# Optimization experiments

Hardware: AMD Instinct MI355X
Metric: run time of the kernel (lower is better)

## Reference

```python
import jax, jax.numpy as jnp
import numpy as np

B, C, D = 8192, 10000, 128
CLAMP_MIN, CLAMP_MAX = 1e-12, 1e12


def setup_inputs() -> dict:
    key = jax.random.key(0)
    k1, k2, k3 = jax.random.split(key, 3)
    x = jax.random.normal(k1, (B, D), dtype=jnp.float32)
    labels = jax.random.randint(k2, (B,), 0, C, dtype=jnp.int64)
    centers = jax.random.normal(k3, (C, D), dtype=jnp.float32)
    lr = jnp.array([0.1], dtype=jnp.float32)
    return {"x": x, "labels": labels, "centers": centers, "lr": lr}


def reference(x, labels, centers, lr):
    b, d = x.shape
    c = centers.shape[0]
    # --- vectorized center update (replaces double python loop) ---
    # A_j = count_j * centers[j] - sum_{i: labels_i==j} x_i ; delta_j = A_j / (1 + count_j)
    counts = jax.ops.segment_sum(jnp.ones((b,), dtype=x.dtype), labels, num_segments=c)  # [C]
    sum_x = jax.ops.segment_sum(x, labels, num_segments=c)                               # [C, D]
    delta = (counts[:, None] * centers - sum_x) / (1.0 + counts[:, None])
    centers = centers - lr * delta
    # --- squared euclidean distance matrix [B, C] ---
    distmat = (
        jnp.sum(x * x, axis=1, keepdims=True)
        + jnp.sum(centers * centers, axis=1)[None, :]
        - 2.0 * (x @ centers.T)
    )
    git = 1.0 / (1.0 + distmat)
    # gather own-class entries (replaces per-sample mask loop)
    lab = labels[:, None]
    center_vals = jnp.take_along_axis(distmat, lab, axis=1)[:, 0]          # [B]
    git_vals = jnp.sum(git, axis=1) - jnp.take_along_axis(git, lab, axis=1)[:, 0]
    center_loss = jnp.mean(jnp.clip(center_vals, CLAMP_MIN, CLAMP_MAX))
    git_loss = jnp.mean(jnp.clip(git_vals, CLAMP_MIN, CLAMP_MAX))
    return (center_loss, git_loss)
```

## Files before the change

### kernel.cpp

```cpp
#include <hip/hip_runtime.h>
#include <hip/hip_bf16.h>

#define B_ 8192
#define C_ 10000
#define D_ 128
#define CPAD 10112
#define NPADC 112
#define NT_TOT 158
#define NSTRIP 16
#define STRIPW 10

typedef float f32x4 __attribute__((ext_vector_type(4)));
typedef short s16x8 __attribute__((ext_vector_type(8)));

typedef const __attribute__((address_space(1))) uint32_t gu32;
typedef __attribute__((address_space(3))) uint32_t lu32;


__global__ void scatter_xprep(const float* __restrict__ x, const int* __restrict__ labels,
                              float* __restrict__ counts, float* __restrict__ sumx,
                              float* __restrict__ xnorm, __hip_bfloat16* __restrict__ xb) {
    int tid = threadIdx.x;
    int w = tid >> 6, lane = tid & 63;
    int i = blockIdx.x * 4 + w;
    int l = labels[i];
    float2 v = *(const float2*)&x[i * D_ + lane * 2];
    atomicAdd(&sumx[l * D_ + lane * 2], v.x);
    atomicAdd(&sumx[l * D_ + lane * 2 + 1], v.y);
    if (lane == 0) atomicAdd(&counts[l], 1.0f);
    __hip_bfloat162 p;
    p.x = __float2bfloat16(v.x);
    p.y = __float2bfloat16(v.y);
    *(__hip_bfloat162*)&xb[i * D_ + lane * 2] = p;
    float s = v.x * v.x + v.y * v.y;
    #pragma unroll
    for (int m = 1; m < 64; m <<= 1) s += __shfl_xor(s, m);
    if (lane == 0) xnorm[i] = s;
}

__global__ void center_update(const float* __restrict__ centers, const float* __restrict__ counts,
                              float* __restrict__ sumx_cnew, float* __restrict__ cnorm,
                              __hip_bfloat16* __restrict__ cb, const float* __restrict__ lr) {
    int tid = threadIdx.x;
    int w = tid >> 6, lane = tid & 63;
    int c = blockIdx.x * 4 + w;
    if (c >= C_) {
        *(uint*)&cb[c * D_ + lane * 2] = 0u;
        if (lane == 0) cnorm[c] = 0.0f;
        return;
    }
    float cnt = counts[c];
    float lrv = lr[0];
    float2 cv = *(const float2*)&centers[c * D_ + lane * 2];
    float2 sx = *(const float2*)&sumx_cnew[c * D_ + lane * 2];
    float inv = 1.0f / (1.0f + cnt);
    float nx = cv.x - lrv * (cnt * cv.x - sx.x) * inv;
    float ny = cv.y - lrv * (cnt * cv.y - sx.y) * inv;
    float2 nn = {nx, ny};
    *(float2*)&sumx_cnew[c * D_ + lane * 2] = nn;
    __hip_bfloat162 p;
    p.x = __float2bfloat16(nx);
    p.y = __float2bfloat16(ny);
    *(__hip_bfloat162*)&cb[c * D_ + lane * 2] = p;
    float s = nx * nx + ny * ny;
    #pragma unroll
    for (int m = 1; m < 64; m <<= 1) s += __shfl_xor(s, m);
    if (lane == 0) cnorm[c] = s;
}

__global__ void center_vals_k(const float* __restrict__ x, const int* __restrict__ labels,
                              const float* __restrict__ cnew, float* __restrict__ cent_val) {
    int tid = threadIdx.x;
    int w = tid >> 6, lane = tid & 63;
    int i = blockIdx.x * 4 + w;
    int l = labels[i];
    float2 a = *(const float2*)&x[i * D_ + lane * 2];
    float2 c = *(const float2*)&cnew[l * D_ + lane * 2];
    float dx = a.x - c.x, dy = a.y - c.y;
    float s = dx * dx + dy * dy;
    #pragma unroll
    for (int m = 1; m < 64; m <<= 1) s += __shfl_xor(s, m);
    if (lane == 0) cent_val[i] = s;
}

__global__ void __launch_bounds__(512)
gemm_git(const __hip_bfloat16* __restrict__ xb, const __hip_bfloat16* __restrict__ cb,
         const float* __restrict__ xnorm, const float* __restrict__ cnorm,
         float* __restrict__ git_row) {
    __shared__ char ldsB[2][16384];

    int tid = threadIdx.x;
    int w = tid >> 6, lane = tid & 63;
    int lr_ = lane & 15, lg = lane >> 4;
    int strip = blockIdx.x;
    int bm = blockIdx.y;
    int row0 = bm * 512 + w * 64;
    int bn0 = strip * STRIPW;
    int nt = (strip == NSTRIP - 1) ? (NT_TOT - bn0) : STRIPW;

    const s16x8* gx = (const s16x8*)xb;

    s16x8 af[4][4];
    #pragma unroll
    for (int kk = 0; kk < 4; kk++)
        #pragma unroll
        for (int f = 0; f < 4; f++)
            af[kk][f] = gx[(row0 + f * 16 + lr_) * 16 + kk * 4 + lg];

    float xn1[4][4];
    #pragma unroll
    for (int fm = 0; fm < 4; fm++)
        #pragma unroll
        for (int r = 0; r < 4; r++)
            xn1[fm][r] = 1.0f + xnorm[row0 + fm * 16 + lg * 4 + r];

    float gitsum[4][4] = {};

    const char* gB = (const char*)cb;
    int sr0 = tid >> 4,          sc0 = (tid & 15) ^ (sr0 & 7);
    int sr1 = (tid + 512) >> 4,  sc1 = ((tid + 512) & 15) ^ (sr1 & 7);
    size_t goff0 = (size_t)(sr0 * 16 + sc0) * 16;
    size_t goff1 = (size_t)(sr1 * 16 + sc1) * 16;

    auto stage = [&](int t, int buf) {
        const char* base = gB + (size_t)(bn0 + t) * 64 * 256;
        __builtin_amdgcn_global_load_lds((gu32*)(base + goff0),
                                         (lu32*)&ldsB[buf][tid * 16], 16, 0, 0);
        __builtin_amdgcn_global_load_lds((gu32*)(base + goff1),
                                         (lu32*)&ldsB[buf][8192 + tid * 16], 16, 0, 0);
    };

    stage(0, 0);
    __syncthreads();

    int cur = 0;
    for (int t = 0; t < nt; ++t) {
        if (t + 1 < nt) stage(t + 1, cur ^ 1);

        int cb0 = (bn0 + t) * 64;
        float cn[4];
        #pragma unroll
        for (int fn = 0; fn < 4; fn++) cn[fn] = cnorm[cb0 + fn * 16 + lr_];

        f32x4 acc[4][4] = {};
        #pragma unroll
        for (int kk = 0; kk < 4; kk++) {
            s16x8 bfk[4];
            int kc = kk * 4 + lg;
            #pragma unroll
            for (int fn = 0; fn < 4; fn++) {
                int row = fn * 16 + lr_;
                int ch = kc ^ (lr_ & 7);
                bfk[fn] = *(const s16x8*)&ldsB[cur][(row * 16 + ch) * 16];
            }
            #pragma unroll
            for (int fm = 0; fm < 4; fm++)
                #pragma unroll
                for (int fn = 0; fn < 4; fn++)
                    acc[fm][fn] = __builtin_amdgcn_mfma_f32_16x16x32_bf16(af[kk][fm], bfk[fn], acc[fm][fn], 0, 0, 0);
        }

        #pragma unroll
        for (int fm = 0; fm < 4; fm++)
            #pragma unroll
            for (int r = 0; r < 4; r++) {
                float base = xn1[fm][r];
                #pragma unroll
                for (int fp = 0; fp < 4; fp += 2) {
                    float u = base + cn[fp]     - 2.0f * acc[fm][fp][r];
                    float v = base + cn[fp + 1] - 2.0f * acc[fm][fp + 1][r];
                    gitsum[fm][r] += (u + v) * __builtin_amdgcn_rcpf(u * v);
                }
            }

        __syncthreads();
        cur ^= 1;
    }

    #pragma unroll
    for (int fm = 0; fm < 4; fm++)
        #pragma unroll
        for (int r = 0; r < 4; r++) {
            float s = gitsum[fm][r];
            s += __shfl_xor(s, 1); s += __shfl_xor(s, 2);
            s += __shfl_xor(s, 4); s += __shfl_xor(s, 8);
            if (lr_ == 0) atomicAdd(&git_row[row0 + fm * 16 + lg * 4 + r], s);
        }
}

__global__ void final_reduce(const float* __restrict__ cent_val, const float* __restrict__ git_row,
                             const float* __restrict__ xnorm, float* __restrict__ out) {
    int tid = threadIdx.x;
    int w = tid >> 6, lane = tid & 63;
    float cl = 0.0f, gl = 0.0f;
    #pragma unroll
    for (int j = 0; j < 2; j++) {
        int base = (tid * 2 + j) * 4;
        float4 cv = *(const float4*)&cent_val[base];
        float4 gr = *(const float4*)&git_row[base];
        float4 xn = *(const float4*)&xnorm[base];
        float cvs[4] = {cv.x, cv.y, cv.z, cv.w};
        float grs[4] = {gr.x, gr.y, gr.z, gr.w};
        float xns[4] = {xn.x, xn.y, xn.z, xn.w};
        #pragma unroll
        for (int e = 0; e < 4; e++) {
            float c = cvs[e];
            cl += fminf(fmaxf(c, 1e-12f), 1e12f);
            float g = grs[e] - 1.0f / (1.0f + c) - (float)NPADC / (1.0f + xns[e]);
            gl += fminf(fmaxf(g, 1e-12f), 1e12f);
        }
    }
    #pragma unroll
    for (int m = 1; m < 64; m <<= 1) { cl += __shfl_xor(cl, m); gl += __shfl_xor(gl, m); }
    __shared__ float scl[16], sgl[16];
    if (lane == 0) { scl[w] = cl; sgl[w] = gl; }
    __syncthreads();
    if (tid == 0) {
        float a = 0.0f, b = 0.0f;
        #pragma unroll
        for (int k = 0; k < 16; k++) { a += scl[k]; b += sgl[k]; }
        out[0] = a / (float)B_;
        out[1] = b / (float)B_;
    }
}

extern "C" void kernel_launch(void* const* d_in, const int* in_sizes, int n_in,
                              void* d_out, int out_size, void* d_ws, size_t ws_size,
                              hipStream_t stream) {
    const float* x       = (const float*)d_in[0];
    const int*   labels  = (const int*)d_in[1];
    const float* centers = (const float*)d_in[2];
    const float* lr      = (const float*)d_in[3];

    float* ws       = (float*)d_ws;
    float* counts   = ws;
    float* sumx     = ws + 10240;
    float* git_row  = ws + 1290240;
    float* xnorm    = ws + 1298432;
    float* cent_val = ws + 1306624;
    float* cnorm    = ws + 1314816;
    __hip_bfloat16* xb = (__hip_bfloat16*)((char*)d_ws + 5300224);
    __hip_bfloat16* cb = (__hip_bfloat16*)((char*)d_ws + 7397376);
    float* out = (float*)d_out;

    hipMemsetAsync(d_ws, 0, (size_t)1298432 * 4, stream);

    scatter_xprep<<<B_ / 4, 256, 0, stream>>>(x, labels, counts, sumx, xnorm, xb);
    center_update<<<CPAD / 4, 256, 0, stream>>>(centers, counts, sumx, cnorm, cb, lr);
    center_vals_k<<<B_ / 4, 256, 0, stream>>>(x, labels, sumx, cent_val);
    gemm_git<<<dim3(NSTRIP, 16), 512, 0, stream>>>(xb, cb, xnorm, cnorm, git_row);
    final_reduce<<<1, 1024, 0, stream>>>(cent_val, git_row, xnorm, out);
}
```

Measured before the change: 57.58 us.

## Fuse center update with own-class distances and shrink GEMM blocks

Merges the center-update and own-class distance kernels into one launch, with the distance blocks recomputing the updated center directly from centers, counts and sumx. This removes one kernel launch and one round trip through global memory. The GEMM blocks drop from 512 to 256 threads, which doubles the number of blocks on the grid to improve occupancy and load balance. The memset is replaced by a zeroing kernel, and the final reduction is spread over 32 blocks that combine results with atomics, which adds atomic accumulation into the output.

```diff
diff --git a/kernel.cpp b/kernel.cpp
--- a/kernel.cpp
+++ b/kernel.cpp
@@ -9,6 +9,8 @@
 #define NT_TOT 158
 #define NSTRIP 16
 #define STRIPW 10
+#define UPD_BLOCKS 2528
+#define CVAL_BLOCKS 2048
 
 typedef float f32x4 __attribute__((ext_vector_type(4)));
 typedef short s16x8 __attribute__((ext_vector_type(8)));
@@ -16,6 +18,11 @@
 typedef const __attribute__((address_space(1))) uint32_t gu32;
 typedef __attribute__((address_space(3))) uint32_t lu32;
 
+
+__global__ void zero_ws(float4* __restrict__ ws, float* __restrict__ out) {
+    ws[blockIdx.x * 256 + threadIdx.x] = float4{0.f, 0.f, 0.f, 0.f};
+    if (blockIdx.x == 0 && threadIdx.x == 0) { out[0] = 0.f; out[1] = 0.f; }
+}
 
 __global__ void scatter_xprep(const float* __restrict__ x, const int* __restrict__ labels,
                               float* __restrict__ counts, float* __restrict__ sumx,
@@ -38,52 +45,56 @@
     if (lane == 0) xnorm[i] = s;
 }
 
-__global__ void center_update(const float* __restrict__ centers, const float* __restrict__ counts,
-                              float* __restrict__ sumx_cnew, float* __restrict__ cnorm,
-                              __hip_bfloat16* __restrict__ cb, const float* __restrict__ lr) {
+__global__ void upd_cvals(const float* __restrict__ centers, const float* __restrict__ counts,
+                          const float* __restrict__ sumx, float* __restrict__ cnorm,
+                          __hip_bfloat16* __restrict__ cb, const float* __restrict__ lr,
+                          const float* __restrict__ x, const int* __restrict__ labels,
+                          float* __restrict__ cent_val) {
     int tid = threadIdx.x;
     int w = tid >> 6, lane = tid & 63;
-    int c = blockIdx.x * 4 + w;
-    if (c >= C_) {
-        *(uint*)&cb[c * D_ + lane * 2] = 0u;
-        if (lane == 0) cnorm[c] = 0.0f;
-        return;
-    }
-    float cnt = counts[c];
+    int bid = blockIdx.x;
     float lrv = lr[0];
-    float2 cv = *(const float2*)&centers[c * D_ + lane * 2];
-    float2 sx = *(const float2*)&sumx_cnew[c * D_ + lane * 2];
-    float inv = 1.0f / (1.0f + cnt);
-    float nx = cv.x - lrv * (cnt * cv.x - sx.x) * inv;
-    float ny = cv.y - lrv * (cnt * cv.y - sx.y) * inv;
-    float2 nn = {nx, ny};
-    *(float2*)&sumx_cnew[c * D_ + lane * 2] = nn;
-    __hip_bfloat162 p;
-    p.x = __float2bfloat16(nx);
-    p.y = __float2bfloat16(ny);
-    *(__hip_bfloat162*)&cb[c * D_ + lane * 2] = p;
-    float s = nx * nx + ny * ny;
-    #pragma unroll
-    for (int m = 1; m < 64; m <<= 1) s += __shfl_xor(s, m);
-    if (lane == 0) cnorm[c] = s;
-}
-
-__global__ void center_vals_k(const float* __restrict__ x, const int* __restrict__ labels,
-                              const float* __restrict__ cnew, float* __restrict__ cent_val) {
-    int tid = threadIdx.x;
-    int w = tid >> 6, lane = tid & 63;
-    int i = blockIdx.x * 4 + w;
-    int l = labels[i];
-    float2 a = *(const float2*)&x[i * D_ + lane * 2];
-    float2 c = *(const float2*)&cnew[l * D_ + lane * 2];
-    float dx = a.x - c.x, dy = a.y - c.y;
-    float s = dx * dx + dy * dy;
-    #pragma unroll
-    for (int m = 1; m < 64; m <<= 1) s += __shfl_xor(s, m);
-    if (lane == 0) cent_val[i] = s;
-}
-
-__global__ void __launch_bounds__(512)
+
+    if (bid < UPD_BLOCKS) {
+        int c = bid * 4 + w;
+        if (c >= C_) {
+            *(uint*)&cb[c * D_ + lane * 2] = 0u;
+            if (lane == 0) cnorm[c] = 0.0f;
+            return;
+        }
+        float cnt = counts[c];
+        float2 cv = *(const float2*)&centers[c * D_ + lane * 2];
+        float2 sx = *(const float2*)&sumx[c * D_ + lane * 2];
+        float inv = 1.0f / (1.0f + cnt);
+        float nx = cv.x - lrv * (cnt * cv.x - sx.x) * inv;
+        float ny = cv.y - lrv * (cnt * cv.y - sx.y) * inv;
+        __hip_bfloat162 p;
+        p.x = __float2bfloat16(nx);
+        p.y = __float2bfloat16(ny);
+        *(__hip_bfloat162*)&cb[c * D_ + lane * 2] = p;
+        float s = nx * nx + ny * ny;
+        #pragma unroll
+        for (int m = 1; m < 64; m <<= 1) s += __shfl_xor(s, m);
+        if (lane == 0) cnorm[c] = s;
+    } else {
+        int i = (bid - UPD_BLOCKS) * 4 + w;
+        int l = labels[i];
+        float cnt = counts[l];
+        float inv = 1.0f / (1.0f + cnt);
+        float2 a  = *(const float2*)&x[i * D_ + lane * 2];
+        float2 cv = *(const float2*)&centers[l * D_ + lane * 2];
+        float2 sx = *(const float2*)&sumx[l * D_ + lane * 2];
+        float nx = cv.x - lrv * (cnt * cv.x - sx.x) * inv;
+        float ny = cv.y - lrv * (cnt * cv.y - sx.y) * inv;
+        float dx = a.x - nx, dy = a.y - ny;
+        float s = dx * dx + dy * dy;
+        #pragma unroll
+        for (int m = 1; m < 64; m <<= 1) s += __shfl_xor(s, m);
+        if (lane == 0) cent_val[i] = s;
+    }
+}
+
+__global__ void __launch_bounds__(256)
 gemm_git(const __hip_bfloat16* __restrict__ xb, const __hip_bfloat16* __restrict__ cb,
          const float* __restrict__ xnorm, const float* __restrict__ cnorm,
          float* __restrict__ git_row) {
@@ -94,7 +105,7 @@
     int lr_ = lane & 15, lg = lane >> 4;
     int strip = blockIdx.x;
     int bm = blockIdx.y;
-    int row0 = bm * 512 + w * 64;
+    int row0 = bm * 256 + w * 64;
     int bn0 = strip * STRIPW;
     int nt = (strip == NSTRIP - 1) ? (NT_TOT - bn0) : STRIPW;
 
@@ -117,17 +128,20 @@
     float gitsum[4][4] = {};
 
     const char* gB = (const char*)cb;
-    int sr0 = tid >> 4,          sc0 = (tid & 15) ^ (sr0 & 7);
-    int sr1 = (tid + 512) >> 4,  sc1 = ((tid + 512) & 15) ^ (sr1 & 7);
-    size_t goff0 = (size_t)(sr0 * 16 + sc0) * 16;
-    size_t goff1 = (size_t)(sr1 * 16 + sc1) * 16;
+    size_t goff[4];
+    #pragma unroll
+    for (int p = 0; p < 4; p++) {
+        int s = tid + p * 256;
+        int sr = s >> 4, sc = (s & 15) ^ (sr & 7);
+        goff[p] = (size_t)(sr * 16 + sc) * 16;
+    }
 
     auto stage = [&](int t, int buf) {
         const char* base = gB + (size_t)(bn0 + t) * 64 * 256;
-        __builtin_amdgcn_global_load_lds((gu32*)(base + goff0),
-                                         (lu32*)&ldsB[buf][tid * 16], 16, 0, 0);
-        __builtin_amdgcn_global_load_lds((gu32*)(base + goff1),
-                                         (lu32*)&ldsB[buf][8192 + tid * 16], 16, 0, 0);
+        #pragma unroll
+        for (int p = 0; p < 4; p++)
+            __builtin_amdgcn_global_load_lds((gu32*)(base + goff[p]),
+                                             (lu32*)&ldsB[buf][(tid + p * 256) * 16], 16, 0, 0);
     };
 
     stage(0, 0);
@@ -191,36 +205,21 @@
 __global__ void final_reduce(const float* __restrict__ cent_val, const float* __restrict__ git_row,
                              const float* __restrict__ xnorm, float* __restrict__ out) {
     int tid = threadIdx.x;
-    int w = tid >> 6, lane = tid & 63;
-    float cl = 0.0f, gl = 0.0f;
-    #pragma unroll
-    for (int j = 0; j < 2; j++) {
-        int base = (tid * 2 + j) * 4;
-        float4 cv = *(const float4*)&cent_val[base];
-        float4 gr = *(const float4*)&git_row[base];
-        float4 xn = *(const float4*)&xnorm[base];
-        float cvs[4] = {cv.x, cv.y, cv.z, cv.w};
-        float grs[4] = {gr.x, gr.y, gr.z, gr.w};
-        float xns[4] = {xn.x, xn.y, xn.z, xn.w};
-        #pragma unroll
-        for (int e = 0; e < 4; e++) {
-            float c = cvs[e];
-            cl += fminf(fmaxf(c, 1e-12f), 1e12f);
-            float g = grs[e] - 1.0f / (1.0f + c) - (float)NPADC / (1.0f + xns[e]);
-            gl += fminf(fmaxf(g, 1e-12f), 1e12f);
-        }
-    }
+    int i = blockIdx.x * 256 + tid;
+    float c = cent_val[i];
+    float cl = fminf(fmaxf(c, 1e-12f), 1e12f);
+    float g = git_row[i] - 1.0f / (1.0f + c) - (float)NPADC / (1.0f + xnorm[i]);
+    float gl = fminf(fmaxf(g, 1e-12f), 1e12f);
     #pragma unroll
     for (int m = 1; m < 64; m <<= 1) { cl += __shfl_xor(cl, m); gl += __shfl_xor(gl, m); }
-    __shared__ float scl[16], sgl[16];
-    if (lane == 0) { scl[w] = cl; sgl[w] = gl; }
+    __shared__ float scl[4], sgl[4];
+    if ((tid & 63) == 0) { scl[tid >> 6] = cl; sgl[tid >> 6] = gl; }
     __syncthreads();
     if (tid == 0) {
-        float a = 0.0f, b = 0.0f;
-        #pragma unroll
-        for (int k = 0; k < 16; k++) { a += scl[k]; b += sgl[k]; }
-        out[0] = a / (float)B_;
-        out[1] = b / (float)B_;
+        float a = scl[0] + scl[1] + scl[2] + scl[3];
+        float b = sgl[0] + sgl[1] + sgl[2] + sgl[3];
+        atomicAdd(&out[0], a / (float)B_);
+        atomicAdd(&out[1], b / (float)B_);
     }
 }
 
@@ -243,11 +242,10 @@
     __hip_bfloat16* cb = (__hip_bfloat16*)((char*)d_ws + 7397376);
     float* out = (float*)d_out;
 
-    hipMemsetAsync(d_ws, 0, (size_t)1298432 * 4, stream);
-
+    zero_ws<<<1268, 256, 0, stream>>>((float4*)d_ws, out);
     scatter_xprep<<<B_ / 4, 256, 0, stream>>>(x, labels, counts, sumx, xnorm, xb);
-    center_update<<<CPAD / 4, 256, 0, stream>>>(centers, counts, sumx, cnorm, cb, lr);
-    center_vals_k<<<B_ / 4, 256, 0, stream>>>(x, labels, sumx, cent_val);
-    gemm_git<<<dim3(NSTRIP, 16), 512, 0, stream>>>(xb, cb, xnorm, cnorm, git_row);
-    final_reduce<<<1, 1024, 0, stream>>>(cent_val, git_row, xnorm, out);
-}
+    upd_cvals<<<UPD_BLOCKS + CVAL_BLOCKS, 256, 0, stream>>>(centers, counts, sumx, cnorm, cb, lr,
+                                                            x, labels, cent_val);
+    gemm_git<<<dim3(NSTRIP, 32), 256, 0, stream>>>(xb, cb, xnorm, cnorm, git_row);
+    final_reduce<<<32, 256, 0, stream>>>(cent_val, git_row, xnorm, out);
+}
```

After: 59.25 us. 2.9% more time.
